# Performance work log

Measured on AMD Instinct MI355X. Metric: run time of the kernel, lower is better.

The kernel has to match this reference:

```python
import jax, jax.numpy as jnp
import numpy as np

T, N, F = 32, 100000, 2
E = 1600000
H4 = 4 * F  # PyTorch LSTM packs gates i,f,g,o


def setup_inputs() -> dict:
    key = jax.random.key(0)
    ks = jax.random.split(key, 8)
    stdv = 1.0 / np.sqrt(F)
    x = jax.random.normal(ks[0], (T, N, F), dtype=jnp.float32)
    edge_index = jax.random.randint(ks[1], (2, E), 0, N, dtype=jnp.int32)
    mask = jax.random.randint(ks[2], (N,), 0, 2, dtype=jnp.int32).astype(bool)
    labels = jnp.zeros((N,), dtype=jnp.int32)
    edge_weight = jnp.ones((E,), dtype=jnp.float32)
    data = 0  # unused placeholder (pyg Data object in original)
    w_ih = jax.random.uniform(ks[3], (H4, F), minval=-stdv, maxval=stdv, dtype=jnp.float32)
    w_hh = jax.random.uniform(ks[4], (H4, F), minval=-stdv, maxval=stdv, dtype=jnp.float32)
    b_ih = jax.random.uniform(ks[5], (H4,), minval=-stdv, maxval=stdv, dtype=jnp.float32)
    b_hh = jax.random.uniform(ks[6], (H4,), minval=-stdv, maxval=stdv, dtype=jnp.float32)
    return {"x": x, "edge_index": edge_index, "mask": mask, "labels": labels,
            "edge_weight": edge_weight, "data": data,
            "w_ih": w_ih, "w_hh": w_hh, "b_ih": b_ih, "b_hh": b_hh}


def _interpolate(x, src, dst, n_nodes):
    # Iteratively fill zero entries with the mean over neighbors whose node
    # has any nonzero data (matches A[row_no_data,:]=0 edge filtering).
    def cond(carry):
        xx, i = carry
        return jnp.logical_and(jnp.any(xx == 0), i < 20)

    def body(carry):
        xx, i = carry
        has_data = jnp.sum(xx != 0, axis=(0, 2)) > 0            # [N]
        valid = has_data[src].astype(xx.dtype)                   # [E]
        msg = xx[:, src, :] * valid[None, :, None]               # [T,E,F]
        agg = jax.ops.segment_sum(jnp.transpose(msg, (1, 0, 2)), dst,
                                  num_segments=n_nodes)          # [N,T,F]
        cnt = jax.ops.segment_sum(valid, dst, num_segments=n_nodes)  # [N]
        mean = jnp.transpose(agg, (1, 0, 2)) / jnp.where(cnt > 0, cnt, 1.0)[None, :, None]
        return jnp.where(xx == 0, mean, xx), i + 1

    out, _ = jax.lax.while_loop(cond, body, (x, jnp.int32(0)))
    return out


def _lstm(x_seq, w_ih, w_hh, b_ih, b_hh):
    # x_seq: [T, N, F]; single-layer LSTM, hidden size F, gate order i,f,g,o.
    n, h = x_seq.shape[1], w_hh.shape[1]
    def step(carry, xt):
        hp, cp = carry
        g = xt @ w_ih.T + b_ih + hp @ w_hh.T + b_hh              # [N, 4F]
        i_, f_, g_, o_ = jnp.split(g, 4, axis=-1)
        i_ = jax.nn.sigmoid(i_); f_ = jax.nn.sigmoid(f_)
        g_ = jnp.tanh(g_);        o_ = jax.nn.sigmoid(o_)
        c = f_ * cp + i_ * g_
        hh = o_ * jnp.tanh(c)
        return (hh, c), hh
    z = jnp.zeros((n, h), dtype=x_seq.dtype)
    _, out = jax.lax.scan(step, (z, z), x_seq)
    return out


def reference(x, edge_index, mask, labels, edge_weight, data, w_ih, w_hh, b_ih, b_hh):
    masked = jnp.where(mask[None, :, None], x, jnp.zeros((), x.dtype))
    src, dst = edge_index[0], edge_index[1]
    interp_x = _interpolate(masked, src, dst, x.shape[1])
    return _lstm(interp_x, w_ih, w_hh, b_ih, b_hh)
```

## Files before the change

kernel.cpp:

```cpp
#include <hip/hip_runtime.h>
#include <math.h>

#define TT    32
#define NN    100000
#define FF    2
#define ROW   64
#define EE    1600000
#define MAXIT 20
#define LDSROW 66
#define BIGIT (1 << 29)
#define NR    8
#define RNG   (NN / NR)
#define SLOT  28
#define QCAP   131072
#define IQCAP  442368
#define CIDCAP 2048
#define CHUNK  782
#define NWORD  3126

typedef float f32x4 __attribute__((ext_vector_type(4)));
typedef float f32x2 __attribute__((ext_vector_type(2)));

__device__ __forceinline__ float fsig(float x) { return 1.0f / (1.0f + __expf(-x)); }
__device__ __forceinline__ float ftanh(float x) { return 2.0f / (1.0f + __expf(-2.0f * x)) - 1.0f; }

__device__ __forceinline__ bool bit_test(const unsigned int* __restrict__ b, int n) {
    return (b[n >> 5] >> (n & 31)) & 1u;
}

__global__ void k_mt_flags(const float* __restrict__ x, const int* __restrict__ mask,
                           float* __restrict__ xx, int* __restrict__ fill_iter,
                           unsigned int* __restrict__ hzb, unsigned int* __restrict__ hdb,
                           int* __restrict__ cnt_v, int* __restrict__ cidmap,
                           int* __restrict__ icnt, int* __restrict__ qc,
                           int* __restrict__ wl_count) {
    __shared__ float tile[64 * LDSROW];
    __shared__ unsigned int wmH[4], wmD[4];
    const int n0 = blockIdx.x * 64;
    const int tid = threadIdx.x;

    if (tid < 64 && n0 + tid < NN) { cnt_v[n0 + tid] = 0; cidmap[n0 + tid] = 0; }
    if (blockIdx.x == 0) {
        if (tid < 32) wl_count[tid] = 0;
        if (tid >= 32 && tid < 48) qc[tid - 32] = 0;
    }
    if (blockIdx.x < 8) icnt[blockIdx.x * 256 + tid] = 0;

#pragma unroll
    for (int r = 0; r < 16; r++) {
        int flat = r * 256 + tid;
        int t = flat >> 7;
        int col = flat & 127;
        int gcol = n0 * 2 + col;
        if (gcol < NN * FF) {
            int n = n0 + (col >> 1);
            float v = __builtin_nontemporal_load(x + (size_t)t * (NN * FF) + gcol);
            v = mask[n] ? v : 0.0f;
            tile[(col >> 1) * LDSROW + t * 2 + (col & 1)] = v;
        }
    }
    __syncthreads();

    const int lane = tid & 63, w = tid >> 6;
    unsigned int mwave = 0, dwave = 0;
    for (int i = 0; i < 16; i++) {
        int ln = w * 16 + i;
        int n = n0 + ln;
        if (n >= NN) break;
        float v = tile[ln * LDSROW + lane];
        unsigned long long nzm = __ballot(v != 0.0f);
        if (nzm != ~0ull) mwave |= (1u << i);
        if (nzm != 0ull)  dwave |= (1u << i);
        if (lane == 0) fill_iter[n] = (nzm != 0ull) ? 0 : BIGIT;
    }
    if (lane == 0) { wmH[w] = mwave; wmD[w] = dwave; }
    __syncthreads();
    if (tid == 0) {
        hzb[2 * blockIdx.x]     = wmH[0] | (wmH[1] << 16);
        hzb[2 * blockIdx.x + 1] = wmH[2] | (wmH[3] << 16);
        hdb[2 * blockIdx.x]     = wmD[0] | (wmD[1] << 16);
        hdb[2 * blockIdx.x + 1] = wmD[2] | (wmD[3] << 16);
    }

#pragma unroll
    for (int j = 0; j < 4; j++) {
        int flat4 = j * 256 + tid;
        int ln = flat4 >> 4;
        int n = n0 + ln;
        if (n >= NN) continue;
        int off = (flat4 & 15) * 4;
        float4 v;
        v.x = tile[ln * LDSROW + off + 0];
        v.y = tile[ln * LDSROW + off + 1];
        v.z = tile[ln * LDSROW + off + 2];
        v.w = tile[ln * LDSROW + off + 3];
        *(float4*)(xx + (size_t)n * ROW + off) = v;
    }
}

__global__ void k_compact(const int* __restrict__ ei, const unsigned int* __restrict__ hzb,
                          const unsigned int* __restrict__ hdb,
                          int2* __restrict__ vq, int2* __restrict__ iq,
                          int* __restrict__ qc) {
    __shared__ int lcnt[9];
    __shared__ int lbase[9];
    const int tid = threadIdx.x;
    if (tid < 9) lcnt[tid] = 0;
    __syncthreads();
    const int e0 = blockIdx.x * CHUNK;
    const int e1 = min(e0 + CHUNK, EE);
    int rs[4], rd[4], rb[4], rp[4];
#pragma unroll
    for (int i = 0; i < 4; i++) {
        rb[i] = -1;
        int e = e0 + i * 256 + tid;
        if (e < e1) {
            int dst = __builtin_nontemporal_load(ei + EE + e);
            if (bit_test(hzb, dst)) {
                int src = __builtin_nontemporal_load(ei + e);
                int b = bit_test(hdb, src) ? (dst / RNG) : 8;
                rs[i] = src; rd[i] = dst; rb[i] = b;
                rp[i] = atomicAdd(&lcnt[b], 1);
            }
        }
    }
    __syncthreads();
    if (tid < 9) lbase[tid] = atomicAdd(&qc[tid], lcnt[tid]);
    __syncthreads();
#pragma unroll
    for (int i = 0; i < 4; i++) {
        if (rb[i] >= 0) {
            int b = rb[i];
            int p = lbase[b] + rp[i];
            if (b < 8) { if (p < QCAP)  vq[b * QCAP + p] = make_int2(rs[i], rd[i]); }
            else       { if (p < IQCAP) iq[p]            = make_int2(rs[i], rd[i]); }
        }
    }
}

__global__ void k_build(const int2* __restrict__ vq, const int* __restrict__ qc,
                        int* __restrict__ cnt_v, int* __restrict__ slab) {
    const int r = blockIdx.x & 7;
    int n = qc[r]; if (n > QCAP) n = QCAP;
    const int gid = (blockIdx.x >> 3) * blockDim.x + threadIdx.x;
    const int stride = (gridDim.x >> 3) * blockDim.x;
    const int2* q = vq + r * QCAP;
    for (int i = gid; i < n; i += stride) {
        int2 sd = q[i];
        int pos = atomicAdd(&cnt_v[sd.y], 1);
        if (pos < SLOT) slab[sd.y * SLOT + pos] = sd.x;
    }
}

__global__ void k_inv(const int2* __restrict__ iq, const int* __restrict__ qc,
                      const int* __restrict__ cnt_v, int* __restrict__ cidmap,
                      int* __restrict__ icnt, int* __restrict__ islab,
                      int* __restrict__ ncid) {
    int n = qc[8]; if (n > IQCAP) n = IQCAP;
    const int gid = blockIdx.x * blockDim.x + threadIdx.x;
    const int stride = gridDim.x * blockDim.x;
    for (int i = gid; i < n; i += stride) {
        int2 sd = iq[i];
        if (cnt_v[sd.y] != 0) continue;
        int cid = cidmap[sd.y];
        if (cid == 0) {
            int nid = atomicAdd(ncid, 1) + 1;
            int old = atomicCAS(&cidmap[sd.y], 0, nid);
            cid = old ? old : nid;
        }
        if (cid <= CIDCAP) {
            int pos = atomicAdd(&icnt[cid - 1], 1);
            if (pos < SLOT) islab[(cid - 1) * SLOT + pos] = sd.x;
        }
    }
}

__device__ __forceinline__ void gather_node4(int n, int k, int lane, bool zrow,
                                             int vbeg, int vend, const int* __restrict__ vsl,
                                             int ibeg, int iend, const int* __restrict__ isl,
                                             int* __restrict__ fill_iter,
                                             float* __restrict__ xx,
                                             int* __restrict__ wl_next,
                                             int* __restrict__ wl_count) {
    const int g = lane >> 4;
    const int s = lane & 15;
    float ax = 0.f, ay = 0.f, az = 0.f, aw = 0.f, cntv = 0.f;
#pragma unroll 2
    for (int e = vbeg + g; e < vend; e += 4) {
        int src = vsl[e];
        f32x4 v = ((const f32x4*)(xx + (size_t)src * ROW))[s];
        ax += v.x; ay += v.y; az += v.z; aw += v.w; cntv += 1.f;
    }
    for (int e = ibeg + g; e < iend; e += 4) {
        int src = isl[e];
        if (fill_iter[src] < k) {
            f32x4 v = ((const f32x4*)(xx + (size_t)src * ROW))[s];
            ax += v.x; ay += v.y; az += v.z; aw += v.w; cntv += 1.f;
        }
    }
#pragma unroll
    for (int d = 16; d <= 32; d <<= 1) {
        ax += __shfl_xor(ax, d, 64);
        ay += __shfl_xor(ay, d, 64);
        az += __shfl_xor(az, d, 64);
        aw += __shfl_xor(aw, d, 64);
        cntv += __shfl_xor(cntv, d, 64);
    }
    f32x4 own;
    if (zrow) { own.x = 0.f; own.y = 0.f; own.z = 0.f; own.w = 0.f; }
    else        own = ((const f32x4*)(xx + (size_t)n * ROW))[s];
    bool has = cntv > 0.f;
    f32x4 nv;
    nv.x = (own.x == 0.f && has) ? ax / cntv : own.x;
    nv.y = (own.y == 0.f && has) ? ay / cntv : own.y;
    nv.z = (own.z == 0.f && has) ? az / cntv : own.z;
    nv.w = (own.w == 0.f && has) ? aw / cntv : own.w;
    bool allnz = (nv.x != 0.f) & (nv.y != 0.f) & (nv.z != 0.f) & (nv.w != 0.f);
    bool anynz = (nv.x != 0.f) | (nv.y != 0.f) | (nv.z != 0.f) | (nv.w != 0.f);
    unsigned long long ba = __ballot(allnz);
    unsigned long long bn = __ballot(anynz);
    if (g == 0) ((f32x4*)(xx + (size_t)n * ROW))[s] = nv;
    if (lane == 0) {
        if (bn != 0ull && fill_iter[n] > k) fill_iter[n] = k;
        if (ba != ~0ull) {
            int pos = atomicAdd(&wl_count[k], 1);
            wl_next[pos] = n;
        }
    }
}

__global__ void k_gather_first(const unsigned int* __restrict__ hzb,
                               const unsigned int* __restrict__ hdb,
                               const int* __restrict__ cnt_v, const int* __restrict__ slab,
                               int* __restrict__ fill_iter, float* __restrict__ xx,
                               int* __restrict__ wl_next, int* __restrict__ wl_count) {
    const int lane = threadIdx.x & 63;
    int wave = (blockIdx.x * blockDim.x + threadIdx.x) >> 6;
    const int nwaves = (gridDim.x * blockDim.x) >> 6;
    for (int n0 = wave; n0 < NN; n0 += nwaves) {
        int n = __builtin_amdgcn_readfirstlane(n0);
        unsigned int hzw = __builtin_amdgcn_readfirstlane(hzb[n >> 5]);
        if (!((hzw >> (n & 31)) & 1u)) continue;
        int cv = cnt_v[n]; if (cv > SLOT) cv = SLOT;
        unsigned int hdw = __builtin_amdgcn_readfirstlane(hdb[n >> 5]);
        bool zrow = !((hdw >> (n & 31)) & 1u);
        gather_node4(n, 1, lane, zrow, n * SLOT, n * SLOT + cv, slab, 0, 0, slab,
                     fill_iter, xx, wl_next, wl_count);
    }
}

__global__ __launch_bounds__(1024)
void k_gather_rest(int* __restrict__ wl_a, int* __restrict__ wl_b,
                   int* __restrict__ wl_count,
                   const int* __restrict__ cnt_v, const int* __restrict__ cidmap,
                   const int* __restrict__ icnt, const int* __restrict__ islab,
                   const int* __restrict__ slab,
                   int* __restrict__ fill_iter, float* __restrict__ xx) {
    const int lane = threadIdx.x & 63;
    const int wave = threadIdx.x >> 6;
    for (int k = 2; k <= MAXIT; k++) {
        int cnt = atomicAdd(&wl_count[k - 1], 0);
        if (cnt == 0) break;
        int* prev = (k & 1) ? wl_b : wl_a;
        int* next = (k & 1) ? wl_a : wl_b;
        for (int w = wave; w < cnt; w += 16) {
            int n = __builtin_amdgcn_readfirstlane(prev[w]);
            int cv = cnt_v[n]; if (cv > SLOT) cv = SLOT;
            int cid = cidmap[n];
            int ci = 0, ib = 0;
            if (cid > 0 && cid <= CIDCAP) {
                ci = icnt[cid - 1]; if (ci > SLOT) ci = SLOT;
                ib = (cid - 1) * SLOT;
            }
            bool zrow = (__builtin_amdgcn_readfirstlane(fill_iter[n]) == BIGIT);
            gather_node4(n, k, lane, zrow, n * SLOT, n * SLOT + cv, slab,
                         ib, ib + ci, islab,
                         fill_iter, xx, next, wl_count);
        }
        __threadfence();
        __syncthreads();
    }
}

__global__ void k_lstm(const float* __restrict__ xx,
                       const float* __restrict__ wih, const float* __restrict__ whh,
                       const float* __restrict__ bih, const float* __restrict__ bhh,
                       float* __restrict__ out) {
    int n = blockIdx.x * 64 + threadIdx.x;
    if (n >= NN) return;
    float Wi[8][2], Wh[8][2], B[8];
#pragma unroll
    for (int kk = 0; kk < 8; kk++) {
        Wi[kk][0] = wih[kk * 2]; Wi[kk][1] = wih[kk * 2 + 1];
        Wh[kk][0] = whh[kk * 2]; Wh[kk][1] = whh[kk * 2 + 1];
        B[kk] = bih[kk] + bhh[kk];
    }
    f32x4 r4[16];
    const f32x4* row4 = (const f32x4*)(xx + (size_t)n * ROW);
#pragma unroll
    for (int i = 0; i < 16; i++) r4[i] = __builtin_nontemporal_load(row4 + i);

    float h0 = 0.f, h1 = 0.f, c0 = 0.f, c1 = 0.f;
#pragma unroll
    for (int t = 0; t < TT; t++) {
        f32x4 q = r4[t >> 1];
        float x0 = (t & 1) ? q.z : q.x;
        float x1 = (t & 1) ? q.w : q.y;
        float g[8];
#pragma unroll
        for (int kk = 0; kk < 8; kk++)
            g[kk] = B[kk] + Wi[kk][0] * x0 + Wi[kk][1] * x1 + Wh[kk][0] * h0 + Wh[kk][1] * h1;
        float i0 = fsig(g[0]), i1 = fsig(g[1]);
        float f0 = fsig(g[2]), f1 = fsig(g[3]);
        float gg0 = ftanh(g[4]), gg1 = ftanh(g[5]);
        float o0 = fsig(g[6]), o1 = fsig(g[7]);
        c0 = f0 * c0 + i0 * gg0;
        c1 = f1 * c1 + i1 * gg1;
        h0 = o0 * ftanh(c0);
        h1 = o1 * ftanh(c1);
        f32x2 hv; hv.x = h0; hv.y = h1;
        __builtin_nontemporal_store(hv, (f32x2*)(out + (size_t)t * (NN * FF) + n * 2));
    }
}

extern "C" void kernel_launch(void* const* d_in, const int* in_sizes, int n_in,
                              void* d_out, int out_size, void* d_ws, size_t ws_size,
                              hipStream_t stream) {
    const float* x    = (const float*)d_in[0];
    const int*   ei   = (const int*)d_in[1];
    const int*   mask = (const int*)d_in[2];
    const float* wih  = (const float*)d_in[6];
    const float* whh  = (const float*)d_in[7];
    const float* bih  = (const float*)d_in[8];
    const float* bhh  = (const float*)d_in[9];
    float* out = (float*)d_out;

    char* ws = (char*)d_ws;
    float* xx        = (float*)ws;
    int*   fill_iter = (int*)(ws + (size_t)NN * ROW * 4);
    int*   wl_count  = fill_iter + NN;
    unsigned int* hzb = (unsigned int*)(wl_count + 32);
    unsigned int* hdb = hzb + NWORD;

    int*  slab   = (int*)d_out;
    int2* vq     = (int2*)(slab + (size_t)NN * SLOT);
    int2* iq     = vq + 8 * (size_t)QCAP;
    int*  cnt_v  = (int*)(iq + IQCAP);
    int*  cidmap = cnt_v + NN;
    int*  wl_a   = cidmap + NN;
    int*  wl_b   = wl_a + NN;
    int*  icnt   = wl_b + NN;
    int*  islab  = icnt + CIDCAP;
    int*  qc     = islab + CIDCAP * SLOT;

    k_mt_flags<<<(NN + 63) / 64, 256, 0, stream>>>(x, mask, xx, fill_iter, hzb, hdb,
                                                   cnt_v, cidmap, icnt, qc, wl_count);
    k_compact<<<(EE + CHUNK - 1) / CHUNK, 256, 0, stream>>>(ei, hzb, hdb, vq, iq, qc);
    k_build<<<2048, 256, 0, stream>>>(vq, qc, cnt_v, slab);
    k_inv<<<512, 256, 0, stream>>>(iq, qc, cnt_v, cidmap, icnt, islab, qc + 9);
    k_gather_first<<<2048, 256, 0, stream>>>(hzb, hdb, cnt_v, slab, fill_iter, xx,
                                             wl_a, wl_count);
    k_gather_rest<<<1, 1024, 0, stream>>>(wl_a, wl_b, wl_count, cnt_v, cidmap, icnt, islab,
                                          slab, fill_iter, xx);
    k_lstm<<<(NN + 63) / 64, 64, 0, stream>>>(xx, wih, whh, bih, bhh, out);
}
```

Measured before the change: 232.2 us.

## Overlap serial gather tail with LSTM and fuse inverse build into first gather

The inverse-slab build runs in extra blocks of the first-gather kernel, which removes one launch. The first gather marks nodes that still have zeros in a dirty bitmap. In a new combined kernel, block 0 runs the serial later gather iterations and then runs the LSTM for the worklist nodes, while all other blocks run the LSTM for clean nodes at the same time. Scratch buffers move from the output buffer into the workspace when it is large enough, which is what allows the LSTM to write the output concurrently; a third worklist keeps the first worklist intact. The risk is that a single block running the LSTM for many dirty nodes becomes the new serial tail.

```diff
diff --git a/kernel.cpp b/kernel.cpp
--- a/kernel.cpp
+++ b/kernel.cpp
@@ -17,6 +17,7 @@
 #define CIDCAP 2048
 #define CHUNK  782
 #define NWORD  3126
+#define GFB    1792
 
 typedef float f32x4 __attribute__((ext_vector_type(4)));
 typedef float f32x2 __attribute__((ext_vector_type(2)));
@@ -31,6 +32,7 @@
 __global__ void k_mt_flags(const float* __restrict__ x, const int* __restrict__ mask,
                            float* __restrict__ xx, int* __restrict__ fill_iter,
                            unsigned int* __restrict__ hzb, unsigned int* __restrict__ hdb,
+                           unsigned int* __restrict__ dzb,
                            int* __restrict__ cnt_v, int* __restrict__ cidmap,
                            int* __restrict__ icnt, int* __restrict__ qc,
                            int* __restrict__ wl_count) {
@@ -45,6 +47,7 @@
         if (tid >= 32 && tid < 48) qc[tid - 32] = 0;
     }
     if (blockIdx.x < 8) icnt[blockIdx.x * 256 + tid] = 0;
+    if (tid < 2) dzb[2 * blockIdx.x + tid] = 0u;
 
 #pragma unroll
     for (int r = 0; r < 16; r++) {
@@ -116,8 +119,8 @@
         int e = e0 + i * 256 + tid;
         if (e < e1) {
             int dst = __builtin_nontemporal_load(ei + EE + e);
+            int src = __builtin_nontemporal_load(ei + e);
             if (bit_test(hzb, dst)) {
-                int src = __builtin_nontemporal_load(ei + e);
                 int b = bit_test(hdb, src) ? (dst / RNG) : 8;
                 rs[i] = src; rd[i] = dst; rb[i] = b;
                 rp[i] = atomicAdd(&lcnt[b], 1);
@@ -152,36 +155,14 @@
     }
 }
 
-__global__ void k_inv(const int2* __restrict__ iq, const int* __restrict__ qc,
-                      const int* __restrict__ cnt_v, int* __restrict__ cidmap,
-                      int* __restrict__ icnt, int* __restrict__ islab,
-                      int* __restrict__ ncid) {
-    int n = qc[8]; if (n > IQCAP) n = IQCAP;
-    const int gid = blockIdx.x * blockDim.x + threadIdx.x;
-    const int stride = gridDim.x * blockDim.x;
-    for (int i = gid; i < n; i += stride) {
-        int2 sd = iq[i];
-        if (cnt_v[sd.y] != 0) continue;
-        int cid = cidmap[sd.y];
-        if (cid == 0) {
-            int nid = atomicAdd(ncid, 1) + 1;
-            int old = atomicCAS(&cidmap[sd.y], 0, nid);
-            cid = old ? old : nid;
-        }
-        if (cid <= CIDCAP) {
-            int pos = atomicAdd(&icnt[cid - 1], 1);
-            if (pos < SLOT) islab[(cid - 1) * SLOT + pos] = sd.x;
-        }
-    }
-}
-
 __device__ __forceinline__ void gather_node4(int n, int k, int lane, bool zrow,
                                              int vbeg, int vend, const int* __restrict__ vsl,
                                              int ibeg, int iend, const int* __restrict__ isl,
                                              int* __restrict__ fill_iter,
                                              float* __restrict__ xx,
                                              int* __restrict__ wl_next,
-                                             int* __restrict__ wl_count) {
+                                             int* __restrict__ wl_count,
+                                             unsigned int* __restrict__ dzb) {
     const int g = lane >> 4;
     const int s = lane & 15;
     float ax = 0.f, ay = 0.f, az = 0.f, aw = 0.f, cntv = 0.f;
@@ -225,18 +206,43 @@
         if (ba != ~0ull) {
             int pos = atomicAdd(&wl_count[k], 1);
             wl_next[pos] = n;
-        }
-    }
-}
-
-__global__ void k_gather_first(const unsigned int* __restrict__ hzb,
-                               const unsigned int* __restrict__ hdb,
-                               const int* __restrict__ cnt_v, const int* __restrict__ slab,
-                               int* __restrict__ fill_iter, float* __restrict__ xx,
-                               int* __restrict__ wl_next, int* __restrict__ wl_count) {
+            if (dzb) atomicOr(&dzb[n >> 5], 1u << (n & 31));
+        }
+    }
+}
+
+__global__ void k_gf_inv(const unsigned int* __restrict__ hzb,
+                         const unsigned int* __restrict__ hdb,
+                         const int* __restrict__ cnt_v, const int* __restrict__ slab,
+                         int* __restrict__ fill_iter, float* __restrict__ xx,
+                         int* __restrict__ wl_next, int* __restrict__ wl_count,
+                         unsigned int* __restrict__ dzb,
+                         const int2* __restrict__ iq, const int* __restrict__ qc,
+                         int* __restrict__ cidmap, int* __restrict__ icnt,
+                         int* __restrict__ islab, int* __restrict__ ncid) {
+    if (blockIdx.x >= GFB) {
+        int n = qc[8]; if (n > IQCAP) n = IQCAP;
+        const int gid = (blockIdx.x - GFB) * blockDim.x + threadIdx.x;
+        const int stride = 256 * blockDim.x;
+        for (int i = gid; i < n; i += stride) {
+            int2 sd = iq[i];
+            if (cnt_v[sd.y] != 0) continue;
+            int cid = cidmap[sd.y];
+            if (cid == 0) {
+                int nid = atomicAdd(ncid, 1) + 1;
+                int old = atomicCAS(&cidmap[sd.y], 0, nid);
+                cid = old ? old : nid;
+            }
+            if (cid <= CIDCAP) {
+                int pos = atomicAdd(&icnt[cid - 1], 1);
+                if (pos < SLOT) islab[(cid - 1) * SLOT + pos] = sd.x;
+            }
+        }
+        return;
+    }
     const int lane = threadIdx.x & 63;
     int wave = (blockIdx.x * blockDim.x + threadIdx.x) >> 6;
-    const int nwaves = (gridDim.x * blockDim.x) >> 6;
+    const int nwaves = (GFB * blockDim.x) >> 6;
     for (int n0 = wave; n0 < NN; n0 += nwaves) {
         int n = __builtin_amdgcn_readfirstlane(n0);
         unsigned int hzw = __builtin_amdgcn_readfirstlane(hzb[n >> 5]);
@@ -245,13 +251,103 @@
         unsigned int hdw = __builtin_amdgcn_readfirstlane(hdb[n >> 5]);
         bool zrow = !((hdw >> (n & 31)) & 1u);
         gather_node4(n, 1, lane, zrow, n * SLOT, n * SLOT + cv, slab, 0, 0, slab,
-                     fill_iter, xx, wl_next, wl_count);
-    }
+                     fill_iter, xx, wl_next, wl_count, dzb);
+    }
+}
+
+__device__ __forceinline__ void lstm_node(int n, const float* __restrict__ xx,
+                                          const float* __restrict__ wih,
+                                          const float* __restrict__ whh,
+                                          const float* __restrict__ bih,
+                                          const float* __restrict__ bhh,
+                                          float* __restrict__ out) {
+    float Wi[8][2], Wh[8][2], B[8];
+#pragma unroll
+    for (int kk = 0; kk < 8; kk++) {
+        Wi[kk][0] = wih[kk * 2]; Wi[kk][1] = wih[kk * 2 + 1];
+        Wh[kk][0] = whh[kk * 2]; Wh[kk][1] = whh[kk * 2 + 1];
+        B[kk] = bih[kk] + bhh[kk];
+    }
+    f32x4 r4[16];
+    const f32x4* row4 = (const f32x4*)(xx + (size_t)n * ROW);
+#pragma unroll
+    for (int i = 0; i < 16; i++) r4[i] = __builtin_nontemporal_load(row4 + i);
+
+    float h0 = 0.f, h1 = 0.f, c0 = 0.f, c1 = 0.f;
+#pragma unroll
+    for (int t = 0; t < TT; t++) {
+        f32x4 q = r4[t >> 1];
+        float x0 = (t & 1) ? q.z : q.x;
+        float x1 = (t & 1) ? q.w : q.y;
+        float g[8];
+#pragma unroll
+        for (int kk = 0; kk < 8; kk++)
+            g[kk] = B[kk] + Wi[kk][0] * x0 + Wi[kk][1] * x1 + Wh[kk][0] * h0 + Wh[kk][1] * h1;
+        float i0 = fsig(g[0]), i1 = fsig(g[1]);
+        float f0 = fsig(g[2]), f1 = fsig(g[3]);
+        float gg0 = ftanh(g[4]), gg1 = ftanh(g[5]);
+        float o0 = fsig(g[6]), o1 = fsig(g[7]);
+        c0 = f0 * c0 + i0 * gg0;
+        c1 = f1 * c1 + i1 * gg1;
+        h0 = o0 * ftanh(c0);
+        h1 = o1 * ftanh(c1);
+        f32x2 hv; hv.x = h0; hv.y = h1;
+        __builtin_nontemporal_store(hv, (f32x2*)(out + (size_t)t * (NN * FF) + n * 2));
+    }
+}
+
+__global__ void k_rest_lstm(int* __restrict__ wl_a, int* __restrict__ wl_b,
+                            int* __restrict__ wl_c,
+                            int* __restrict__ wl_count,
+                            const int* __restrict__ cnt_v, const int* __restrict__ cidmap,
+                            const int* __restrict__ icnt, const int* __restrict__ islab,
+                            const int* __restrict__ slab,
+                            int* __restrict__ fill_iter, float* __restrict__ xx,
+                            const unsigned int* __restrict__ dzb,
+                            const float* __restrict__ wih, const float* __restrict__ whh,
+                            const float* __restrict__ bih, const float* __restrict__ bhh,
+                            float* __restrict__ out) {
+    if (blockIdx.x == 0) {
+        const int lane = threadIdx.x & 63;
+        const int wave = threadIdx.x >> 6;
+        for (int k = 2; k <= MAXIT; k++) {
+            int cnt = atomicAdd(&wl_count[k - 1], 0);
+            if (cnt == 0) break;
+            int* prev = (k == 2) ? wl_a : ((k & 1) ? wl_b : wl_c);
+            int* next = (k & 1) ? wl_c : wl_b;
+            for (int w = wave; w < cnt; w += 4) {
+                int n = __builtin_amdgcn_readfirstlane(prev[w]);
+                int cv = cnt_v[n]; if (cv > SLOT) cv = SLOT;
+                int cid = cidmap[n];
+                int ci = 0, ib = 0;
+                if (cid > 0 && cid <= CIDCAP) {
+                    ci = icnt[cid - 1]; if (ci > SLOT) ci = SLOT;
+                    ib = (cid - 1) * SLOT;
+                }
+                bool zrow = (__builtin_amdgcn_readfirstlane(fill_iter[n]) == BIGIT);
+                gather_node4(n, k, lane, zrow, n * SLOT, n * SLOT + cv, slab,
+                             ib, ib + ci, islab,
+                             fill_iter, xx, next, wl_count, (unsigned int*)0);
+            }
+            __threadfence();
+            __syncthreads();
+        }
+        __threadfence();
+        __syncthreads();
+        int cnt1 = wl_count[1]; if (cnt1 > NN) cnt1 = NN;
+        for (int i = threadIdx.x; i < cnt1; i += blockDim.x)
+            lstm_node(wl_a[i], xx, wih, whh, bih, bhh, out);
+        return;
+    }
+    int n = (blockIdx.x - 1) * 256 + threadIdx.x;
+    if (n >= NN) return;
+    if (bit_test(dzb, n)) return;
+    lstm_node(n, xx, wih, whh, bih, bhh, out);
 }
 
 __global__ __launch_bounds__(1024)
 void k_gather_rest(int* __restrict__ wl_a, int* __restrict__ wl_b,
-                   int* __restrict__ wl_count,
+                   int* __restrict__ wl_c, int* __restrict__ wl_count,
                    const int* __restrict__ cnt_v, const int* __restrict__ cidmap,
                    const int* __restrict__ icnt, const int* __restrict__ islab,
                    const int* __restrict__ slab,
@@ -261,8 +357,8 @@
     for (int k = 2; k <= MAXIT; k++) {
         int cnt = atomicAdd(&wl_count[k - 1], 0);
         if (cnt == 0) break;
-        int* prev = (k & 1) ? wl_b : wl_a;
-        int* next = (k & 1) ? wl_a : wl_b;
+        int* prev = (k == 2) ? wl_a : ((k & 1) ? wl_b : wl_c);
+        int* next = (k & 1) ? wl_c : wl_b;
         for (int w = wave; w < cnt; w += 16) {
             int n = __builtin_amdgcn_readfirstlane(prev[w]);
             int cv = cnt_v[n]; if (cv > SLOT) cv = SLOT;
@@ -275,52 +371,20 @@
             bool zrow = (__builtin_amdgcn_readfirstlane(fill_iter[n]) == BIGIT);
             gather_node4(n, k, lane, zrow, n * SLOT, n * SLOT + cv, slab,
                          ib, ib + ci, islab,
-                         fill_iter, xx, next, wl_count);
+                         fill_iter, xx, next, wl_count, (unsigned int*)0);
         }
         __threadfence();
         __syncthreads();
     }
 }
 
-__global__ void k_lstm(const float* __restrict__ xx,
-                       const float* __restrict__ wih, const float* __restrict__ whh,
-                       const float* __restrict__ bih, const float* __restrict__ bhh,
-                       float* __restrict__ out) {
+__global__ void k_lstm_all(const float* __restrict__ xx,
+                           const float* __restrict__ wih, const float* __restrict__ whh,
+                           const float* __restrict__ bih, const float* __restrict__ bhh,
+                           float* __restrict__ out) {
     int n = blockIdx.x * 64 + threadIdx.x;
     if (n >= NN) return;
-    float Wi[8][2], Wh[8][2], B[8];
-#pragma unroll
-    for (int kk = 0; kk < 8; kk++) {
-        Wi[kk][0] = wih[kk * 2]; Wi[kk][1] = wih[kk * 2 + 1];
-        Wh[kk][0] = whh[kk * 2]; Wh[kk][1] = whh[kk * 2 + 1];
-        B[kk] = bih[kk] + bhh[kk];
-    }
-    f32x4 r4[16];
-    const f32x4* row4 = (const f32x4*)(xx + (size_t)n * ROW);
-#pragma unroll
-    for (int i = 0; i < 16; i++) r4[i] = __builtin_nontemporal_load(row4 + i);
-
-    float h0 = 0.f, h1 = 0.f, c0 = 0.f, c1 = 0.f;
-#pragma unroll
-    for (int t = 0; t < TT; t++) {
-        f32x4 q = r4[t >> 1];
-        float x0 = (t & 1) ? q.z : q.x;
-        float x1 = (t & 1) ? q.w : q.y;
-        float g[8];
-#pragma unroll
-        for (int kk = 0; kk < 8; kk++)
-            g[kk] = B[kk] + Wi[kk][0] * x0 + Wi[kk][1] * x1 + Wh[kk][0] * h0 + Wh[kk][1] * h1;
-        float i0 = fsig(g[0]), i1 = fsig(g[1]);
-        float f0 = fsig(g[2]), f1 = fsig(g[3]);
-        float gg0 = ftanh(g[4]), gg1 = ftanh(g[5]);
-        float o0 = fsig(g[6]), o1 = fsig(g[7]);
-        c0 = f0 * c0 + i0 * gg0;
-        c1 = f1 * c1 + i1 * gg1;
-        h0 = o0 * ftanh(c0);
-        h1 = o1 * ftanh(c1);
-        f32x2 hv; hv.x = h0; hv.y = h1;
-        __builtin_nontemporal_store(hv, (f32x2*)(out + (size_t)t * (NN * FF) + n * 2));
-    }
+    lstm_node(n, xx, wih, whh, bih, bhh, out);
 }
 
 extern "C" void kernel_launch(void* const* d_in, const int* in_sizes, int n_in,
@@ -341,26 +405,43 @@
     int*   wl_count  = fill_iter + NN;
     unsigned int* hzb = (unsigned int*)(wl_count + 32);
     unsigned int* hdb = hzb + NWORD;
-
-    int*  slab   = (int*)d_out;
+    unsigned int* dzb = hdb + NWORD;
+
+    size_t fixed = (size_t)NN * ROW * 4 + (size_t)NN * 4 + 32 * 4 + 3ull * NWORD * 4;
+    size_t scratch = (size_t)NN * SLOT * 4 + 8ull * QCAP * 8 + (size_t)IQCAP * 8
+                   + 5ull * NN * 4 + (size_t)CIDCAP * 4 + (size_t)CIDCAP * SLOT * 4 + 256;
+    bool big_ws = ws_size >= fixed + scratch + 64;
+    char* scb = big_ws ? (ws + fixed) : (char*)d_out;
+    scb = (char*)(((size_t)scb + 15) & ~(size_t)15);
+
+    int*  slab   = (int*)scb;
     int2* vq     = (int2*)(slab + (size_t)NN * SLOT);
     int2* iq     = vq + 8 * (size_t)QCAP;
     int*  cnt_v  = (int*)(iq + IQCAP);
     int*  cidmap = cnt_v + NN;
     int*  wl_a   = cidmap + NN;
     int*  wl_b   = wl_a + NN;
-    int*  icnt   = wl_b + NN;
+    int*  wl_c   = wl_b + NN;
+    int*  icnt   = wl_c + NN;
     int*  islab  = icnt + CIDCAP;
     int*  qc     = islab + CIDCAP * SLOT;
 
-    k_mt_flags<<<(NN + 63) / 64, 256, 0, stream>>>(x, mask, xx, fill_iter, hzb, hdb,
+    k_mt_flags<<<(NN + 63) / 64, 256, 0, stream>>>(x, mask, xx, fill_iter, hzb, hdb, dzb,
                                                    cnt_v, cidmap, icnt, qc, wl_count);
     k_compact<<<(EE + CHUNK - 1) / CHUNK, 256, 0, stream>>>(ei, hzb, hdb, vq, iq, qc);
     k_build<<<2048, 256, 0, stream>>>(vq, qc, cnt_v, slab);
-    k_inv<<<512, 256, 0, stream>>>(iq, qc, cnt_v, cidmap, icnt, islab, qc + 9);
-    k_gather_first<<<2048, 256, 0, stream>>>(hzb, hdb, cnt_v, slab, fill_iter, xx,
-                                             wl_a, wl_count);
-    k_gather_rest<<<1, 1024, 0, stream>>>(wl_a, wl_b, wl_count, cnt_v, cidmap, icnt, islab,
-                                          slab, fill_iter, xx);
-    k_lstm<<<(NN + 63) / 64, 64, 0, stream>>>(xx, wih, whh, bih, bhh, out);
-}
+    k_gf_inv<<<GFB + 256, 256, 0, stream>>>(hzb, hdb, cnt_v, slab, fill_iter, xx,
+                                            wl_a, wl_count, dzb,
+                                            iq, qc, cidmap, icnt, islab, qc + 9);
+    if (big_ws) {
+        k_rest_lstm<<<1 + (NN + 255) / 256, 256, 0, stream>>>(wl_a, wl_b, wl_c, wl_count,
+                                                              cnt_v, cidmap, icnt, islab,
+                                                              slab, fill_iter, xx, dzb,
+                                                              wih, whh, bih, bhh, out);
+    } else {
+        k_gather_rest<<<1, 1024, 0, stream>>>(wl_a, wl_b, wl_c, wl_count,
+                                              cnt_v, cidmap, icnt, islab,
+                                              slab, fill_iter, xx);
+        k_lstm_all<<<(NN + 63) / 64, 64, 0, stream>>>(xx, wih, whh, bih, bhh, out);
+    }
+}
```

New measurement: 235.5 us. No clear change (+1.4%).

## Fuse inverse-adjacency build into first gather kernel and move scratch to workspace

Applied to the files above, without the earlier changes.

Merges k_inv into the first gather launch by giving extra blocks the inverse-queue work, so both run concurrently and one launch is removed. It also adds a third worklist buffer so that wl_a, which the first gather fills, is never overwritten. Scratch buffers now go in the workspace instead of the output buffer when the workspace is large enough, and the src load in compaction is issued unconditionally. The LSTM kernel gets launch bounds. The fused kernel is only correct if the gather blocks never read the inverse slab, which appears to hold for the first iteration.

```diff
diff --git a/kernel.cpp b/kernel.cpp
--- a/kernel.cpp
+++ b/kernel.cpp
@@ -17,6 +17,7 @@
 #define CIDCAP 2048
 #define CHUNK  782
 #define NWORD  3126
+#define GFB    1792
 
 typedef float f32x4 __attribute__((ext_vector_type(4)));
 typedef float f32x2 __attribute__((ext_vector_type(2)));
@@ -116,8 +117,8 @@
         int e = e0 + i * 256 + tid;
         if (e < e1) {
             int dst = __builtin_nontemporal_load(ei + EE + e);
+            int src = __builtin_nontemporal_load(ei + e);
             if (bit_test(hzb, dst)) {
-                int src = __builtin_nontemporal_load(ei + e);
                 int b = bit_test(hdb, src) ? (dst / RNG) : 8;
                 rs[i] = src; rd[i] = dst; rb[i] = b;
                 rp[i] = atomicAdd(&lcnt[b], 1);
@@ -149,29 +150,6 @@
         int2 sd = q[i];
         int pos = atomicAdd(&cnt_v[sd.y], 1);
         if (pos < SLOT) slab[sd.y * SLOT + pos] = sd.x;
-    }
-}
-
-__global__ void k_inv(const int2* __restrict__ iq, const int* __restrict__ qc,
-                      const int* __restrict__ cnt_v, int* __restrict__ cidmap,
-                      int* __restrict__ icnt, int* __restrict__ islab,
-                      int* __restrict__ ncid) {
-    int n = qc[8]; if (n > IQCAP) n = IQCAP;
-    const int gid = blockIdx.x * blockDim.x + threadIdx.x;
-    const int stride = gridDim.x * blockDim.x;
-    for (int i = gid; i < n; i += stride) {
-        int2 sd = iq[i];
-        if (cnt_v[sd.y] != 0) continue;
-        int cid = cidmap[sd.y];
-        if (cid == 0) {
-            int nid = atomicAdd(ncid, 1) + 1;
-            int old = atomicCAS(&cidmap[sd.y], 0, nid);
-            cid = old ? old : nid;
-        }
-        if (cid <= CIDCAP) {
-            int pos = atomicAdd(&icnt[cid - 1], 1);
-            if (pos < SLOT) islab[(cid - 1) * SLOT + pos] = sd.x;
-        }
     }
 }
 
@@ -229,14 +207,37 @@
     }
 }
 
-__global__ void k_gather_first(const unsigned int* __restrict__ hzb,
-                               const unsigned int* __restrict__ hdb,
-                               const int* __restrict__ cnt_v, const int* __restrict__ slab,
-                               int* __restrict__ fill_iter, float* __restrict__ xx,
-                               int* __restrict__ wl_next, int* __restrict__ wl_count) {
+__global__ void k_gf_inv(const unsigned int* __restrict__ hzb,
+                         const unsigned int* __restrict__ hdb,
+                         const int* __restrict__ cnt_v, const int* __restrict__ slab,
+                         int* __restrict__ fill_iter, float* __restrict__ xx,
+                         int* __restrict__ wl_next, int* __restrict__ wl_count,
+                         const int2* __restrict__ iq, const int* __restrict__ qc,
+                         int* __restrict__ cidmap, int* __restrict__ icnt,
+                         int* __restrict__ islab, int* __restrict__ ncid) {
+    if (blockIdx.x >= GFB) {
+        int n = qc[8]; if (n > IQCAP) n = IQCAP;
+        const int gid = (blockIdx.x - GFB) * blockDim.x + threadIdx.x;
+        const int stride = 256 * blockDim.x;
+        for (int i = gid; i < n; i += stride) {
+            int2 sd = iq[i];
+            if (cnt_v[sd.y] != 0) continue;
+            int cid = cidmap[sd.y];
+            if (cid == 0) {
+                int nid = atomicAdd(ncid, 1) + 1;
+                int old = atomicCAS(&cidmap[sd.y], 0, nid);
+                cid = old ? old : nid;
+            }
+            if (cid <= CIDCAP) {
+                int pos = atomicAdd(&icnt[cid - 1], 1);
+                if (pos < SLOT) islab[(cid - 1) * SLOT + pos] = sd.x;
+            }
+        }
+        return;
+    }
     const int lane = threadIdx.x & 63;
     int wave = (blockIdx.x * blockDim.x + threadIdx.x) >> 6;
-    const int nwaves = (gridDim.x * blockDim.x) >> 6;
+    const int nwaves = (GFB * blockDim.x) >> 6;
     for (int n0 = wave; n0 < NN; n0 += nwaves) {
         int n = __builtin_amdgcn_readfirstlane(n0);
         unsigned int hzw = __builtin_amdgcn_readfirstlane(hzb[n >> 5]);
@@ -251,7 +252,7 @@
 
 __global__ __launch_bounds__(1024)
 void k_gather_rest(int* __restrict__ wl_a, int* __restrict__ wl_b,
-                   int* __restrict__ wl_count,
+                   int* __restrict__ wl_c, int* __restrict__ wl_count,
                    const int* __restrict__ cnt_v, const int* __restrict__ cidmap,
                    const int* __restrict__ icnt, const int* __restrict__ islab,
                    const int* __restrict__ slab,
@@ -261,8 +262,8 @@
     for (int k = 2; k <= MAXIT; k++) {
         int cnt = atomicAdd(&wl_count[k - 1], 0);
         if (cnt == 0) break;
-        int* prev = (k & 1) ? wl_b : wl_a;
-        int* next = (k & 1) ? wl_a : wl_b;
+        int* prev = (k == 2) ? wl_a : ((k & 1) ? wl_b : wl_c);
+        int* next = (k & 1) ? wl_c : wl_b;
         for (int w = wave; w < cnt; w += 16) {
             int n = __builtin_amdgcn_readfirstlane(prev[w]);
             int cv = cnt_v[n]; if (cv > SLOT) cv = SLOT;
@@ -282,10 +283,11 @@
     }
 }
 
-__global__ void k_lstm(const float* __restrict__ xx,
-                       const float* __restrict__ wih, const float* __restrict__ whh,
-                       const float* __restrict__ bih, const float* __restrict__ bhh,
-                       float* __restrict__ out) {
+__global__ __launch_bounds__(64, 1)
+void k_lstm_all(const float* __restrict__ xx,
+                const float* __restrict__ wih, const float* __restrict__ whh,
+                const float* __restrict__ bih, const float* __restrict__ bhh,
+                float* __restrict__ out) {
     int n = blockIdx.x * 64 + threadIdx.x;
     if (n >= NN) return;
     float Wi[8][2], Wh[8][2], B[8];
@@ -342,14 +344,22 @@
     unsigned int* hzb = (unsigned int*)(wl_count + 32);
     unsigned int* hdb = hzb + NWORD;
 
-    int*  slab   = (int*)d_out;
+    size_t fixed = (size_t)NN * ROW * 4 + (size_t)NN * 4 + 32 * 4 + 2ull * NWORD * 4;
+    size_t scratch = (size_t)NN * SLOT * 4 + 8ull * QCAP * 8 + (size_t)IQCAP * 8
+                   + 5ull * NN * 4 + (size_t)CIDCAP * 4 + (size_t)CIDCAP * SLOT * 4 + 256;
+    bool big_ws = ws_size >= fixed + scratch + 64;
+    char* scb = big_ws ? (ws + fixed) : (char*)d_out;
+    scb = (char*)(((size_t)scb + 15) & ~(size_t)15);
+
+    int*  slab   = (int*)scb;
     int2* vq     = (int2*)(slab + (size_t)NN * SLOT);
     int2* iq     = vq + 8 * (size_t)QCAP;
     int*  cnt_v  = (int*)(iq + IQCAP);
     int*  cidmap = cnt_v + NN;
     int*  wl_a   = cidmap + NN;
     int*  wl_b   = wl_a + NN;
-    int*  icnt   = wl_b + NN;
+    int*  wl_c   = wl_b + NN;
+    int*  icnt   = wl_c + NN;
     int*  islab  = icnt + CIDCAP;
     int*  qc     = islab + CIDCAP * SLOT;
 
@@ -357,10 +367,11 @@
                                                    cnt_v, cidmap, icnt, qc, wl_count);
     k_compact<<<(EE + CHUNK - 1) / CHUNK, 256, 0, stream>>>(ei, hzb, hdb, vq, iq, qc);
     k_build<<<2048, 256, 0, stream>>>(vq, qc, cnt_v, slab);
-    k_inv<<<512, 256, 0, stream>>>(iq, qc, cnt_v, cidmap, icnt, islab, qc + 9);
-    k_gather_first<<<2048, 256, 0, stream>>>(hzb, hdb, cnt_v, slab, fill_iter, xx,
-                                             wl_a, wl_count);
-    k_gather_rest<<<1, 1024, 0, stream>>>(wl_a, wl_b, wl_count, cnt_v, cidmap, icnt, islab,
+    k_gf_inv<<<GFB + 256, 256, 0, stream>>>(hzb, hdb, cnt_v, slab, fill_iter, xx,
+                                            wl_a, wl_count,
+                                            iq, qc, cidmap, icnt, islab, qc + 9);
+    k_gather_rest<<<1, 1024, 0, stream>>>(wl_a, wl_b, wl_c, wl_count,
+                                          cnt_v, cidmap, icnt, islab,
                                           slab, fill_iter, xx);
-    k_lstm<<<(NN + 63) / 64, 64, 0, stream>>>(xx, wih, whh, bih, bhh, out);
-}
+    k_lstm_all<<<(NN + 63) / 64, 64, 0, stream>>>(xx, wih, whh, bih, bhh, out);
+}
```

Result: faster. 223.5 us, median of 2 (-3.7%).
